# Kernel tuning notes

Measured on AMD Instinct MI355X. Metric: run time of the kernel, lower is better.

Reference implementation:

```python
import jax, jax.numpy as jnp
import numpy as np
from jax.scipy.special import logsumexp

VOCAB, EMB, HID, S, B = 50000, 300, 512, 200, 64
N_TAGS = 64
N_LABELS = N_TAGS + 2  # +start/+stop
START, STOP = N_LABELS - 2, N_LABELS - 1
MAX_NORM = 6.0


def setup_inputs() -> dict:
    key = jax.random.key(0)
    ks = jax.random.split(key, 10)
    data = jax.random.randint(ks[0], (B, S), 0, VOCAB)
    lengths = jnp.sort(jax.random.randint(ks[1], (B,), 1, S + 1))[::-1]
    lengths = lengths.at[0].set(S)  # longest sequence fills the padded length
    labels = jax.random.randint(ks[2], (B, S), 0, N_TAGS)
    emb_table = jax.random.normal(ks[3], (VOCAB, EMB), jnp.float32)
    s_ih = 1.0 / np.sqrt(HID)
    W_ih = jax.random.uniform(ks[4], (4 * HID, EMB), jnp.float32, -s_ih, s_ih)
    W_hh = jax.random.uniform(ks[5], (4 * HID, HID), jnp.float32, -s_ih, s_ih)
    b = jax.random.uniform(ks[6], (4 * HID,), jnp.float32, -s_ih, s_ih)  # b_ih+b_hh fused
    s_fc = 1.0 / np.sqrt(HID)
    W_fc = jax.random.uniform(ks[7], (N_LABELS, HID), jnp.float32, -s_fc, s_fc)
    b_fc = jax.random.uniform(ks[8], (N_LABELS,), jnp.float32, -s_fc, s_fc)
    transitions = jax.random.normal(ks[9], (N_LABELS, N_LABELS), jnp.float32)
    return {"data": data, "lengths": lengths, "labels": labels,
            "emb_table": emb_table, "W_ih": W_ih, "W_hh": W_hh, "b": b,
            "W_fc": W_fc, "b_fc": b_fc, "transitions": transitions}


def _embed(emb_table, data):
    # nn.Embedding max_norm=6: renorm rows whose L2 norm exceeds 6
    norms = jnp.linalg.norm(emb_table, axis=1, keepdims=True)
    scale = jnp.minimum(1.0, MAX_NORM / jnp.maximum(norms, 1e-7))
    return (emb_table * scale)[data]  # [B,S,E]


def _lstm(emb, W_ih, W_hh, b):
    # gate order i,f,g,o (PyTorch). emb: [B,S,E]
    x_proj = jnp.einsum('bse,ge->bsg', emb, W_ih) + b  # [B,S,4H]
    def step(carry, xt):
        h, c = carry
        gates = xt + h @ W_hh.T
        i, f, g, o = jnp.split(gates, 4, axis=-1)
        c = jax.nn.sigmoid(f) * c + jax.nn.sigmoid(i) * jnp.tanh(g)
        h = jax.nn.sigmoid(o) * jnp.tanh(c)
        return (h, c), h
    h0 = jnp.zeros((emb.shape[0], HID), emb.dtype)
    _, hs = jax.lax.scan(step, (h0, h0), jnp.swapaxes(x_proj, 0, 1))
    return jnp.swapaxes(hs, 0, 1)  # [B,S,H]


def _crf_norm(logits, lengths, transitions):
    # forward algorithm: alpha_nxt[b,i] = LSE_j(trans[i,j]+alpha[b,j]) + logit[b,i]
    Bsz = logits.shape[0]
    alpha0 = jnp.full((Bsz, N_LABELS), -10000.0).at[:, START].set(0.0)
    def step(alpha, inp):
        logit, t = inp
        alpha_nxt = logsumexp(transitions[None, :, :] + alpha[:, None, :], axis=2) + logit
        alpha = jnp.where((t < lengths)[:, None], alpha_nxt, alpha)
        return alpha, None
    alpha, _ = jax.lax.scan(step, alpha0, (jnp.swapaxes(logits, 0, 1), jnp.arange(logits.shape[1])))
    return logsumexp(alpha + transitions[STOP][None, :], axis=1)  # [B]


def _transition_score(labels, lengths, transitions):
    Bsz, Sl = labels.shape
    ext = jnp.concatenate([jnp.full((Bsz, 1), START, labels.dtype), labels,
                           jnp.full((Bsz, 1), STOP, labels.dtype)], axis=1)  # [B,S+2]
    pos = jnp.arange(Sl + 2)
    ext = jnp.where(pos[None, :] < (lengths + 1)[:, None], ext, STOP)
    trn = transitions[ext[:, 1:], ext[:, :-1]]  # [B,S+1]
    mask = (jnp.arange(Sl + 1)[None, :] < (lengths + 1)[:, None]).astype(trn.dtype)
    return (trn * mask).sum(1)


def _features_score(feats, labels, lengths):
    scr = jnp.take_along_axis(feats, labels[:, :, None], axis=2)[:, :, 0]
    mask = (jnp.arange(labels.shape[1])[None, :] < lengths[:, None]).astype(scr.dtype)
    return (scr * mask).sum(1)


def reference(data, lengths, labels, emb_table, W_ih, W_hh, b, W_fc, b_fc, transitions):
    emb = _embed(emb_table, data)                # dropout: eval mode (identity)
    h = _lstm(emb, W_ih, W_hh, b)
    feats = h @ W_fc.T + b_fc                    # BatchNorm2d(1): eval mode (identity)
    norm = _crf_norm(feats, lengths, transitions)
    seq_score = _transition_score(labels, lengths, transitions) + _features_score(feats, labels, lengths)
    return norm - seq_score                      # per-sentence neg log-likelihood [B]
```

## Files before the change

### kernel.cpp

```cpp
#include <hip/hip_runtime.h>
#include <hip/hip_bf16.h>

typedef __attribute__((ext_vector_type(8))) short short8_t;
typedef __attribute__((ext_vector_type(4))) float f32x4_t;

__device__ __forceinline__ unsigned short f2bf(float f) {
    unsigned u = __float_as_uint(f);
    unsigned r = (u + 0x7FFFu + ((u >> 16) & 1u)) >> 16;
    return (unsigned short)r;
}
__device__ __forceinline__ float bf2f(unsigned short u) {
    return __uint_as_float(((unsigned)u) << 16);
}
__device__ __forceinline__ float bflo(unsigned u) { return __uint_as_float(u << 16); }
__device__ __forceinline__ float bfhi(unsigned u) { return __uint_as_float(u & 0xFFFF0000u); }
__device__ __forceinline__ float sigm(float x) { return 1.f / (1.f + __expf(-x)); }
__device__ __forceinline__ float tanhfast(float x) {
    x = fminf(fmaxf(x, -15.f), 15.f);
    float e = __expf(2.f * x);
    return (e - 1.f) / (e + 1.f);
}

__device__ __forceinline__ void ld4_sc1(const void* p, uint4& a) {
    asm volatile("global_load_dwordx4 %0, %1, off sc1\n\ts_waitcnt vmcnt(0)"
                 : "=v"(a) : "v"(p) : "memory");
}
__device__ __forceinline__ void st1_sc1(void* p, unsigned v) {
    asm volatile("global_store_dword %0, %1, off sc1" :: "v"(p), "v"(v) : "memory");
}
__device__ __forceinline__ unsigned ld1_sc1(const void* p) {
    unsigned v;
    asm volatile("global_load_dword %0, %1, off sc1\n\ts_waitcnt vmcnt(0)"
                 : "=v"(v) : "v"(p) : "memory");
    return v;
}

#define BATCH 64
#define SEQ 200
#define HID 512
#define G4 2048
#define NLAB 66
#define START_L 64
#define STOP_L 65
#define KPAD 320


__global__ __launch_bounds__(256) void embed_k(const int* __restrict__ data,
                                               const float* __restrict__ emb,
                                               unsigned short* __restrict__ A) {
    int w = threadIdx.x >> 6, l = threadIdx.x & 63;
    int tok = blockIdx.x * 4 + w;
    int s = tok >> 6, b = tok & 63;
    int row = data[b * SEQ + s];
    const float* src = emb + (size_t)row * 300;
    float vals[5];
    float ss = 0.f;
#pragma unroll
    for (int u = 0; u < 5; u++) {
        int e = l + u * 64;
        float v = (e < 300) ? src[e] : 0.f;
        vals[u] = v;
        ss += v * v;
    }
#pragma unroll
    for (int off = 1; off < 64; off <<= 1) ss += __shfl_xor(ss, off);
    float nrm = sqrtf(ss);
    float scale = fminf(1.f, 6.f / fmaxf(nrm, 1e-7f));
    unsigned short* dst = A + (size_t)tok * KPAD;
#pragma unroll
    for (int u = 0; u < 5; u++) {
        int e = l + u * 64;
        dst[e] = (e < 300) ? f2bf(vals[u] * scale) : (unsigned short)0;
    }
}

__global__ void convw_k(const float* __restrict__ W, unsigned short* __restrict__ Wb) {
    int idx = blockIdx.x * blockDim.x + threadIdx.x;
    if (idx < G4 * KPAD) {
        int r = idx / KPAD, k = idx % KPAD;
        Wb[idx] = (k < 300) ? f2bf(W[r * 300 + k]) : (unsigned short)0;
    }
}

template <int MODE>
__global__ __launch_bounds__(256) void gemm_k(const unsigned short* __restrict__ Abf,
                                              const float* __restrict__ Af32,
                                              const unsigned short* __restrict__ Bbf,
                                              unsigned short* __restrict__ Cbf,
                                              float* __restrict__ Cf32,
                                              const float* __restrict__ bias) {
    constexpr int KTOT = (MODE == 0) ? KPAD : HID;
    constexpr int NKT = KTOT / 64;
    const int bm = (MODE == 0) ? (blockIdx.x & 15) : 0;
    const int bn = (MODE == 0) ? (blockIdx.x >> 4) : blockIdx.x;
    const int m0 = bm * 128, n0 = bn * 128;
    __shared__ unsigned short Al[128 * 72];
    __shared__ unsigned short Bl[128 * 72];
    const int tid = threadIdx.x;
    const int w = tid >> 6, l = tid & 63;
    const int wr = w >> 1, wc = w & 1;
    f32x4_t acc[4][4];
#pragma unroll
    for (int i = 0; i < 4; i++)
#pragma unroll
        for (int j = 0; j < 4; j++) {
            acc[i][j].x = 0.f; acc[i][j].y = 0.f; acc[i][j].z = 0.f; acc[i][j].w = 0.f;
        }

    for (int kt = 0; kt < NKT; kt++) {
        int row = tid >> 1, half = tid & 1;
        int kbase = kt * 64 + half * 32;
        if constexpr (MODE == 0) {
            const unsigned short* src = Abf + (size_t)(m0 + row) * KPAD + kbase;
#pragma unroll
            for (int q = 0; q < 4; q++)
                *(short8_t*)&Al[row * 72 + half * 32 + q * 8] = *(const short8_t*)(src + q * 8);
        } else {
            if (row < NLAB) {
                const float* src = Af32 + (size_t)row * HID + kbase;
#pragma unroll
                for (int q = 0; q < 4; q++) {
                    short8_t o;
#pragma unroll
                    for (int x = 0; x < 8; x++) o[x] = (short)f2bf(src[q * 8 + x]);
                    *(short8_t*)&Al[row * 72 + half * 32 + q * 8] = o;
                }
            } else {
                short8_t z = {0, 0, 0, 0, 0, 0, 0, 0};
#pragma unroll
                for (int q = 0; q < 4; q++)
                    *(short8_t*)&Al[row * 72 + half * 32 + q * 8] = z;
            }
        }
        if constexpr (MODE == 0) {
            const unsigned short* src = Bbf + (size_t)(n0 + row) * KTOT + kbase;
#pragma unroll
            for (int q = 0; q < 4; q++)
                *(short8_t*)&Bl[row * 72 + half * 32 + q * 8] = *(const short8_t*)(src + q * 8);
        } else {
            int t0 = bn * 2;
            int tt = tid >> 7, gg = (tid >> 4) & 7, dq = tid & 15;
#pragma unroll
            for (int dd = 0; dd < 4; dd++) {
                int d = dq * 4 + dd;
                uint4 vv = *(const uint4*)((const char*)Bbf +
                    ((((size_t)(t0 + tt) * 8 + gg) * 8 + kt) * 1024 + (size_t)d * 16));
#pragma unroll
                for (int lb = 0; lb < 8; lb++) {
                    unsigned u = vv[lb >> 1];
                    Bl[(tt * 64 + gg * 8 + lb) * 72 + d] =
                        (unsigned short)((lb & 1) ? (u >> 16) : (u & 0xFFFFu));
                }
            }
        }
        __syncthreads();
#pragma unroll
        for (int kk2 = 0; kk2 < 2; kk2++) {
            short8_t af[4], bfv[4];
#pragma unroll
            for (int i = 0; i < 4; i++)
                af[i] = *(const short8_t*)&Al[(wr * 64 + i * 16 + (l & 15)) * 72 + kk2 * 32 + (l >> 4) * 8];
#pragma unroll
            for (int j = 0; j < 4; j++)
                bfv[j] = *(const short8_t*)&Bl[(wc * 64 + j * 16 + (l & 15)) * 72 + kk2 * 32 + (l >> 4) * 8];
#pragma unroll
            for (int i = 0; i < 4; i++)
#pragma unroll
                for (int j = 0; j < 4; j++)
                    acc[i][j] = __builtin_amdgcn_mfma_f32_16x16x32_bf16(af[i], bfv[j], acc[i][j], 0, 0, 0);
        }
        __syncthreads();
    }
#pragma unroll
    for (int i = 0; i < 4; i++)
#pragma unroll
        for (int j = 0; j < 4; j++)
#pragma unroll
            for (int r = 0; r < 4; r++) {
                int m = m0 + wr * 64 + i * 16 + (l >> 4) * 4 + r;
                int n = n0 + wc * 64 + j * 16 + (l & 15);
                float v = acc[i][j][r];
                if constexpr (MODE == 0) {
                    int tt = n >> 6, gg = (n >> 3) & 7, lb = n & 7;
                    Cbf[((size_t)(gg * 2048 + m)) * 1600 + tt * 8 + lb] = f2bf(v);
                } else {
                    if (m < NLAB) {
                        int b = n & 63, s = n >> 6;
                        Cf32[((size_t)b * SEQ + s) * NLAB + m] = v + bias[m];
                    }
                }
            }
}

__global__ __launch_bounds__(512, 1) void lstm_k(const float* __restrict__ Whh,
                                                 const float* __restrict__ bvec,
                                                 const unsigned short* __restrict__ X,
                                                 unsigned short* __restrict__ HS,
                                                 unsigned* __restrict__ flags) {
    const int g = blockIdx.x & 7;
    const int j = blockIdx.x >> 3;
    const int tid = threadIdx.x;
    const int w = tid >> 6, l = tid & 63;

    __shared__ unsigned short hB[16][520];
    __shared__ float gates_l[256][10];
    __shared__ float bias_s[256];

    const int q = w >> 1, ebase = (w & 1) * 32;
    short8_t wreg[2][16];
#pragma unroll
    for (int mt = 0; mt < 2; mt++)
#pragma unroll
        for (int ks = 0; ks < 16; ks++) {
            int gr = q * 512 + j * 64 + ebase + mt * 16 + (l & 15);
            const float* wp = Whh + (size_t)gr * HID + ks * 32 + (l >> 4) * 8;
            float4 f0 = *(const float4*)wp;
            float4 f1 = *(const float4*)(wp + 4);
            short8_t o;
            o[0] = (short)f2bf(f0.x); o[1] = (short)f2bf(f0.y);
            o[2] = (short)f2bf(f0.z); o[3] = (short)f2bf(f0.w);
            o[4] = (short)f2bf(f1.x); o[5] = (short)f2bf(f1.y);
            o[6] = (short)f2bf(f1.z); o[7] = (short)f2bf(f1.w);
            wreg[mt][ks] = o;
        }
    for (int idx = tid; idx < 16 * 520; idx += 512) ((unsigned short*)hB)[idx] = 0;
    if (tid < 256) bias_s[tid] = bvec[(tid >> 6) * 512 + j * 64 + (tid & 63)];
    __syncthreads();

    unsigned* gfl = flags + g * 32;
    unsigned* HSu = (unsigned*)HS;
    const int e = tid >> 3, lb = tid & 7;
    float cpriv = 0.f;

    for (int t = 0; t < SEQ; t++) {
        float xv[4];
#pragma unroll
        for (int q2 = 0; q2 < 4; q2++)
            xv[q2] = bf2f(X[((size_t)(g * 2048 + q2 * 512 + j * 64 + e)) * 1600 + t * 8 + lb]);

        if (t > 0) {
            if (w == 0) {
                unsigned v = ld1_sc1(&gfl[(l & 7) * 4]);
                while (!__all((int)(v >= (unsigned)t))) {
                    __builtin_amdgcn_s_sleep(2);
                    v = ld1_sc1(&gfl[(l & 7) * 4]);
                }
            }
            __syncthreads();
            const unsigned* hsrc = HSu + ((size_t)(t - 1) * 8 + g) * 2048 + tid * 4;
            uint4 va;
            ld4_sc1(hsrc, va);
#pragma unroll
            for (int i = 0; i < 4; i++) {
                unsigned u = va[i];
                hB[2 * i][tid] = (unsigned short)(u & 0xFFFFu);
                hB[2 * i + 1][tid] = (unsigned short)(u >> 16);
            }
        }
        __syncthreads();

        f32x4_t a0 = {0.f, 0.f, 0.f, 0.f}, a1 = {0.f, 0.f, 0.f, 0.f};
#pragma unroll
        for (int ks = 0; ks < 16; ks++) {
            short8_t bf = *(const short8_t*)&hB[l & 15][ks * 32 + (l >> 4) * 8];
            a0 = __builtin_amdgcn_mfma_f32_16x16x32_bf16(wreg[0][ks], bf, a0, 0, 0, 0);
            a1 = __builtin_amdgcn_mfma_f32_16x16x32_bf16(wreg[1][ks], bf, a1, 0, 0, 0);
        }
        if ((l & 15) < 8) {
            int rb = w * 32 + (l >> 4) * 4;
#pragma unroll
            for (int r = 0; r < 4; r++) gates_l[rb + r][l & 7] = a0[r];
#pragma unroll
            for (int r = 0; r < 4; r++) gates_l[rb + 16 + r][l & 7] = a1[r];
        }
        __syncthreads();

        float pre[4];
#pragma unroll
        for (int q2 = 0; q2 < 4; q2++)
            pre[q2] = gates_l[q2 * 64 + e][lb] + bias_s[q2 * 64 + e] + xv[q2];
        float ig = sigm(pre[0]);
        float fg = sigm(pre[1]);
        float gg = tanhfast(pre[2]);
        float og = sigm(pre[3]);
        float c = fg * cpriv + ig * gg;
        cpriv = c;
        float h = og * tanhfast(c);
        unsigned short hb = f2bf(h);
        unsigned short hb1 = (unsigned short)__shfl_xor((int)hb, 1);
        if ((tid & 1) == 0) {
            unsigned pk = (unsigned)hb | ((unsigned)hb1 << 16);
            unsigned* seg = HSu + ((size_t)t * 8 + g) * 2048 + j * 256;
            st1_sc1(&seg[tid >> 1], pk);
        }
        asm volatile("s_waitcnt vmcnt(0)" ::: "memory");
        __syncthreads();
        if (tid == 0) st1_sc1(&gfl[j * 4], (unsigned)(t + 1));
    }
}

__global__ __launch_bounds__(320) void crf_k(const float* __restrict__ F,
                                             const float* __restrict__ trans,
                                             const int* __restrict__ labels,
                                             const int* __restrict__ lengths,
                                             float* __restrict__ out) {
    const int b = blockIdx.x;
    const int tid = threadIdx.x;
    __shared__ float tl[NLAB * NLAB];
    __shared__ float alpha[2][68];
    __shared__ float fbuf[68];
    __shared__ float red[8];
    __shared__ float norm_s;
    for (int i = tid; i < NLAB * NLAB; i += 320) tl[i] = trans[i];
    const int L = lengths[b];
    const int ii = tid >> 2, jq = tid & 3;
    const int j0 = (jq < 2) ? jq * 17 : 34 + (jq - 2) * 16;
    const int jn = (jq < 2) ? 17 : 16;
    if (tid < NLAB) alpha[0][tid] = (tid == START_L) ? 0.f : -10000.f;
    __syncthreads();
    int p = 0;
    for (int t = 0; t < L; t++) {
        if (tid < NLAB) fbuf[tid] = F[((size_t)b * SEQ + t) * NLAB + tid];
        __syncthreads();
        if (ii < NLAB) {
            float v[17];
            float m = -3.0e38f;
#pragma unroll
            for (int u = 0; u < 17; u++) {
                float x = (u < jn) ? tl[ii * NLAB + j0 + u] + alpha[p][j0 + u] : -3.0e38f;
                v[u] = x;
                m = fmaxf(m, x);
            }
            m = fmaxf(m, __shfl_xor(m, 1));
            m = fmaxf(m, __shfl_xor(m, 2));
            float s = 0.f;
#pragma unroll
            for (int u = 0; u < 17; u++) s += __expf(v[u] - m);
            s += __shfl_xor(s, 1);
            s += __shfl_xor(s, 2);
            if (jq == 0) alpha[p ^ 1][ii] = m + __logf(s) + fbuf[ii];
        }
        __syncthreads();
        p ^= 1;
    }
    if (tid < 64) {
        float v0 = alpha[p][tid] + tl[STOP_L * NLAB + tid];
        float v1 = (tid + 64 < NLAB) ? alpha[p][tid + 64] + tl[STOP_L * NLAB + tid + 64] : -3.0e38f;
        float m = fmaxf(v0, v1);
#pragma unroll
        for (int off = 1; off < 64; off <<= 1) m = fmaxf(m, __shfl_xor(m, off));
        float s = __expf(v0 - m) + ((tid + 64 < NLAB) ? __expf(v1 - m) : 0.f);
#pragma unroll
        for (int off = 1; off < 64; off <<= 1) s += __shfl_xor(s, off);
        if (tid == 0) norm_s = m + __logf(s);
    }
    float local = 0.f;
    const int* lab = labels + (size_t)b * SEQ;
    for (int k = tid; k < L; k += 320) {
        int lk = lab[k];
        int prev = (k == 0) ? START_L : lab[k - 1];
        local += tl[lk * NLAB + prev] + F[((size_t)b * SEQ + k) * NLAB + lk];
    }
    if (tid == 0) local += tl[STOP_L * NLAB + lab[L - 1]];
#pragma unroll
    for (int off = 1; off < 64; off <<= 1) local += __shfl_xor(local, off);
    if ((tid & 63) == 0) red[tid >> 6] = local;
    __syncthreads();
    if (tid == 0) {
        float tot = red[0] + red[1] + red[2] + red[3] + red[4];
        out[b] = norm_s - tot;
    }
}

extern "C" void kernel_launch(void* const* d_in, const int* in_sizes, int n_in,
                              void* d_out, int out_size, void* d_ws, size_t ws_size,
                              hipStream_t stream) {
    const int* data = (const int*)d_in[0];
    const int* lengths = (const int*)d_in[1];
    const int* labels = (const int*)d_in[2];
    const float* emb = (const float*)d_in[3];
    const float* W_ih = (const float*)d_in[4];
    const float* W_hh = (const float*)d_in[5];
    const float* bvec = (const float*)d_in[6];
    const float* W_fc = (const float*)d_in[7];
    const float* b_fc = (const float*)d_in[8];
    const float* trans = (const float*)d_in[9];
    float* out = (float*)d_out;

    const size_t oA = 0;
    const size_t oW = 8192000;
    const size_t oX = 9502720;
    const size_t oHS = 61931520;
    const size_t oF = 75038720;
    const size_t oC = 78417920;
    const size_t need = 78418944;
    if (ws_size < need) return;

    char* w = (char*)d_ws;
    unsigned short* A = (unsigned short*)(w + oA);
    unsigned short* Wb = (unsigned short*)(w + oW);
    unsigned short* X = (unsigned short*)(w + oX);
    unsigned short* HS = (unsigned short*)(w + oHS);
    float* F = (float*)(w + oF);
    unsigned* flags = (unsigned*)(w + oC);

    hipMemsetAsync(flags, 0, 1024, stream);
    embed_k<<<3200, 256, 0, stream>>>(data, emb, A);
    convw_k<<<2560, 256, 0, stream>>>(W_ih, Wb);
    gemm_k<0><<<1600, 256, 0, stream>>>(Wb, nullptr, A, X, nullptr, nullptr);
    lstm_k<<<64, 512, 0, stream>>>(W_hh, bvec, X, HS, flags);
    gemm_k<1><<<100, 256, 0, stream>>>(nullptr, W_fc, HS, nullptr, F, b_fc);
    crf_k<<<64, 320, 0, stream>>>(F, trans, labels, lengths, out);
}
```

Before: 882.4 us.

## Rewrite CRF forward as single-wave kernel with register-held transition rows

The CRF kernel drops from 320 threads with a 4-way split per label to a single 64-thread wavefront. Each lane keeps its full transition row in registers and the whole sequence of emission scores is preloaded into shared memory. This removes the per-step global load and the extra barrier. Lanes 0-1 also compute the two extra labels serially, which adds a tail to every step. Separately, the LSTM hidden-state shared buffer row stride is padded from 520 to 522 to change the LDS bank mapping.

After: 1.169 ms. 1.33x slower.

```diff
diff --git a/kernel.cpp b/kernel.cpp
--- a/kernel.cpp
+++ b/kernel.cpp
@@ -43,6 +43,7 @@
 #define START_L 64
 #define STOP_L 65
 #define KPAD 320
+#define HBS 522
 
 
 __global__ __launch_bounds__(256) void embed_k(const int* __restrict__ data,
@@ -202,7 +203,7 @@
     const int tid = threadIdx.x;
     const int w = tid >> 6, l = tid & 63;
 
-    __shared__ unsigned short hB[16][520];
+    __shared__ unsigned short hB[16][HBS];
     __shared__ float gates_l[256][10];
     __shared__ float bias_s[256];
 
@@ -223,7 +224,7 @@
             o[6] = (short)f2bf(f1.z); o[7] = (short)f2bf(f1.w);
             wreg[mt][ks] = o;
         }
-    for (int idx = tid; idx < 16 * 520; idx += 512) ((unsigned short*)hB)[idx] = 0;
+    for (int idx = tid; idx < 16 * HBS; idx += 512) ((unsigned short*)hB)[idx] = 0;
     if (tid < 256) bias_s[tid] = bvec[(tid >> 6) * 512 + j * 64 + (tid & 63)];
     __syncthreads();
 
@@ -299,77 +300,98 @@
     }
 }
 
-__global__ __launch_bounds__(320) void crf_k(const float* __restrict__ F,
-                                             const float* __restrict__ trans,
-                                             const int* __restrict__ labels,
-                                             const int* __restrict__ lengths,
-                                             float* __restrict__ out) {
+__global__ __launch_bounds__(64) void crf_k(const float* __restrict__ F,
+                                            const float* __restrict__ trans,
+                                            const int* __restrict__ labels,
+                                            const int* __restrict__ lengths,
+                                            float* __restrict__ out) {
     const int b = blockIdx.x;
-    const int tid = threadIdx.x;
-    __shared__ float tl[NLAB * NLAB];
+    const int l = threadIdx.x;
+    __shared__ float fbuf[SEQ][68];
     __shared__ float alpha[2][68];
-    __shared__ float fbuf[68];
-    __shared__ float red[8];
-    __shared__ float norm_s;
-    for (int i = tid; i < NLAB * NLAB; i += 320) tl[i] = trans[i];
+
     const int L = lengths[b];
-    const int ii = tid >> 2, jq = tid & 3;
-    const int j0 = (jq < 2) ? jq * 17 : 34 + (jq - 2) * 16;
-    const int jn = (jq < 2) ? 17 : 16;
-    if (tid < NLAB) alpha[0][tid] = (tid == START_L) ? 0.f : -10000.f;
+    {
+        const float* src = F + (size_t)b * SEQ * NLAB;
+        for (int t = 0; t < SEQ; t++) {
+            fbuf[t][l] = src[t * NLAB + l];
+            if (l < 2) fbuf[t][64 + l] = src[t * NLAB + 64 + l];
+        }
+    }
+    float trow[NLAB];
+#pragma unroll
+    for (int jj = 0; jj < NLAB; jj++) trow[jj] = trans[l * NLAB + jj];
+    float tstop = trans[STOP_L * NLAB + l];
+    float tstop2 = (l < 2) ? trans[STOP_L * NLAB + 64 + l] : -3.0e38f;
+
+    alpha[0][l] = (l == START_L) ? 0.f : -10000.f;
+    if (l < 2) alpha[0][64 + l] = ((64 + l) == START_L) ? 0.f : -10000.f;
     __syncthreads();
+
     int p = 0;
     for (int t = 0; t < L; t++) {
-        if (tid < NLAB) fbuf[tid] = F[((size_t)b * SEQ + t) * NLAB + tid];
-        __syncthreads();
-        if (ii < NLAB) {
-            float v[17];
-            float m = -3.0e38f;
-#pragma unroll
-            for (int u = 0; u < 17; u++) {
-                float x = (u < jn) ? tl[ii * NLAB + j0 + u] + alpha[p][j0 + u] : -3.0e38f;
-                v[u] = x;
-                m = fmaxf(m, x);
-            }
-            m = fmaxf(m, __shfl_xor(m, 1));
-            m = fmaxf(m, __shfl_xor(m, 2));
-            float s = 0.f;
-#pragma unroll
-            for (int u = 0; u < 17; u++) s += __expf(v[u] - m);
-            s += __shfl_xor(s, 1);
-            s += __shfl_xor(s, 2);
-            if (jq == 0) alpha[p ^ 1][ii] = m + __logf(s) + fbuf[ii];
-        }
+        float v[NLAB];
+        float m0 = -3.0e38f, m1 = -3.0e38f, m2 = -3.0e38f, m3 = -3.0e38f;
+#pragma unroll
+        for (int jj = 0; jj < 64; jj += 4) {
+            v[jj] = trow[jj] + alpha[p][jj];
+            v[jj + 1] = trow[jj + 1] + alpha[p][jj + 1];
+            v[jj + 2] = trow[jj + 2] + alpha[p][jj + 2];
+            v[jj + 3] = trow[jj + 3] + alpha[p][jj + 3];
+            m0 = fmaxf(m0, v[jj]); m1 = fmaxf(m1, v[jj + 1]);
+            m2 = fmaxf(m2, v[jj + 2]); m3 = fmaxf(m3, v[jj + 3]);
+        }
+        v[64] = trow[64] + alpha[p][64];
+        v[65] = trow[65] + alpha[p][65];
+        m0 = fmaxf(m0, v[64]); m1 = fmaxf(m1, v[65]);
+        float m = fmaxf(fmaxf(m0, m1), fmaxf(m2, m3));
+        float s0 = 0.f, s1 = 0.f, s2 = 0.f, s3 = 0.f;
+#pragma unroll
+        for (int jj = 0; jj < 64; jj += 4) {
+            s0 += __expf(v[jj] - m); s1 += __expf(v[jj + 1] - m);
+            s2 += __expf(v[jj + 2] - m); s3 += __expf(v[jj + 3] - m);
+        }
+        s0 += __expf(v[64] - m); s1 += __expf(v[65] - m);
+        float anew = m + __logf((s0 + s1) + (s2 + s3)) + fbuf[t][l];
+
+        float anew2 = 0.f;
+        if (l < 2) {
+            const float* tr2 = trans + (64 + l) * NLAB;
+            float mm = -3.0e38f;
+#pragma unroll
+            for (int jj = 0; jj < NLAB; jj++) mm = fmaxf(mm, tr2[jj] + alpha[p][jj]);
+            float ss = 0.f;
+#pragma unroll
+            for (int jj = 0; jj < NLAB; jj++) ss += __expf(tr2[jj] + alpha[p][jj] - mm);
+            anew2 = mm + __logf(ss) + fbuf[t][64 + l];
+        }
+        alpha[p ^ 1][l] = anew;
+        if (l < 2) alpha[p ^ 1][64 + l] = anew2;
         __syncthreads();
         p ^= 1;
     }
-    if (tid < 64) {
-        float v0 = alpha[p][tid] + tl[STOP_L * NLAB + tid];
-        float v1 = (tid + 64 < NLAB) ? alpha[p][tid + 64] + tl[STOP_L * NLAB + tid + 64] : -3.0e38f;
-        float m = fmaxf(v0, v1);
-#pragma unroll
-        for (int off = 1; off < 64; off <<= 1) m = fmaxf(m, __shfl_xor(m, off));
-        float s = __expf(v0 - m) + ((tid + 64 < NLAB) ? __expf(v1 - m) : 0.f);
-#pragma unroll
-        for (int off = 1; off < 64; off <<= 1) s += __shfl_xor(s, off);
-        if (tid == 0) norm_s = m + __logf(s);
-    }
+
+    float val = alpha[p][l] + tstop;
+    float val2 = (l < 2) ? alpha[p][64 + l] + tstop2 : -3.0e38f;
+    float mloc = fmaxf(val, val2);
+#pragma unroll
+    for (int off = 1; off < 64; off <<= 1) mloc = fmaxf(mloc, __shfl_xor(mloc, off));
+    float sloc = __expf(val - mloc) + ((l < 2) ? __expf(val2 - mloc) : 0.f);
+#pragma unroll
+    for (int off = 1; off < 64; off <<= 1) sloc += __shfl_xor(sloc, off);
+    float norm = mloc + __logf(sloc);
+
     float local = 0.f;
     const int* lab = labels + (size_t)b * SEQ;
-    for (int k = tid; k < L; k += 320) {
+    for (int k = l; k < L; k += 64) {
         int lk = lab[k];
         int prev = (k == 0) ? START_L : lab[k - 1];
-        local += tl[lk * NLAB + prev] + F[((size_t)b * SEQ + k) * NLAB + lk];
-    }
-    if (tid == 0) local += tl[STOP_L * NLAB + lab[L - 1]];
+        local += trans[lk * NLAB + prev] + fbuf[k][lk];
+    }
+    if (l == 0) local += trans[STOP_L * NLAB + lab[L - 1]];
 #pragma unroll
     for (int off = 1; off < 64; off <<= 1) local += __shfl_xor(local, off);
-    if ((tid & 63) == 0) red[tid >> 6] = local;
-    __syncthreads();
-    if (tid == 0) {
-        float tot = red[0] + red[1] + red[2] + red[3] + red[4];
-        out[b] = norm_s - tot;
-    }
+    if (l == 0) out[b] = norm - local;
 }
 
 extern "C" void kernel_launch(void* const* d_in, const int* in_sizes, int n_in,
@@ -410,5 +432,5 @@
     gemm_k<0><<<1600, 256, 0, stream>>>(Wb, nullptr, A, X, nullptr, nullptr);
     lstm_k<<<64, 512, 0, stream>>>(W_hh, bvec, X, HS, flags);
     gemm_k<1><<<100, 256, 0, stream>>>(nullptr, W_fc, HS, nullptr, F, b_fc);
-    crf_k<<<64, 320, 0, stream>>>(F, trans, labels, lengths, out);
-}
+    crf_k<<<64, 64, 0, stream>>>(F, trans, labels, lengths, out);
+}
```
